# Kernel tuning notes

Measured on AMD Instinct MI355X. Metric: run time of the kernel, lower is better.

The kernel has to match this reference:

```python
import jax, jax.numpy as jnp
import numpy as np

HEADS = 16
DIM_HEAD = 64
MAX_REL_POS = 16  # temporal_length


def setup_inputs() -> dict:
    key = jax.random.key(0)
    ks = jax.random.split(key, 8)
    B, T, D = 2048, 16, 1024
    inner = HEADS * DIM_HEAD  # 1024
    w = 0.02  # weight init scale for numerical stability
    return {
        "x": jax.random.normal(ks[0], (B, T, D), jnp.float32),
        "Wq": jax.random.normal(ks[1], (inner, D), jnp.float32) * w,
        "Wk": jax.random.normal(ks[2], (inner, D), jnp.float32) * w,
        "Wv": jax.random.normal(ks[3], (inner, D), jnp.float32) * w,
        "Wo": jax.random.normal(ks[4], (D, inner), jnp.float32) * w,
        "bo": jnp.zeros((D,), jnp.float32),
        "rel_k_table": jax.random.normal(ks[5], (2 * MAX_REL_POS + 1, DIM_HEAD), jnp.float32) * w,
        "rel_v_table": jax.random.normal(ks[6], (2 * MAX_REL_POS + 1, DIM_HEAD), jnp.float32) * w,
    }


def reference(x, Wq, Wk, Wv, Wo, bo, rel_k_table, rel_v_table):
    B, T, D = x.shape
    h, dh = HEADS, DIM_HEAD
    scale = dh ** -0.5

    def split_heads(t):  # [B,T,h*dh] -> [B*h,T,dh]
        return t.reshape(B, T, h, dh).transpose(0, 2, 1, 3).reshape(B * h, T, dh)

    q = split_heads(x @ Wq.T)
    k = split_heads(x @ Wk.T)
    v = split_heads(x @ Wv.T)

    sim = jnp.einsum('bid,bjd->bij', q, k) * scale

    # relative-position bias: idx[i,j] = clip(j-i, -L, L) + L
    r = jnp.arange(T)
    idx = jnp.clip(r[None, :] - r[:, None], -MAX_REL_POS, MAX_REL_POS) + MAX_REL_POS
    k2 = rel_k_table[idx]  # [T,T,dh]
    sim = sim + jnp.einsum('btd,tsd->bts', q, k2) * scale

    attn = jax.nn.softmax(sim, axis=-1)
    out = jnp.einsum('bij,bjd->bid', attn, v)
    v2 = rel_v_table[idx]  # [T,T,dh]
    out = out + jnp.einsum('bts,tsd->btd', attn, v2)

    out = out.reshape(B, h, T, dh).transpose(0, 2, 1, 3).reshape(B, T, h * dh)
    return out @ Wo.T + bo
```

## Files before the change

### kernel.cpp

```cpp
#include <hip/hip_runtime.h>

#define HEADS 16
#define DIM_HEAD 64
#define T_SEQ 16
#define D_MODEL 1024
#define MAX_REL 16

typedef _Float16 half8 __attribute__((ext_vector_type(8)));
typedef float f32x4 __attribute__((ext_vector_type(4)));

__global__ __launch_bounds__(256)
void cvt_f32_f16(const float* __restrict__ in, _Float16* __restrict__ out, int n8) {
  int i = blockIdx.x * blockDim.x + threadIdx.x;
  if (i >= n8) return;
  float4 a = ((const float4*)in)[2 * i];
  float4 b = ((const float4*)in)[2 * i + 1];
  half8 h;
  h[0] = (_Float16)a.x; h[1] = (_Float16)a.y;
  h[2] = (_Float16)a.z; h[3] = (_Float16)a.w;
  h[4] = (_Float16)b.x; h[5] = (_Float16)b.y;
  h[6] = (_Float16)b.z; h[7] = (_Float16)b.w;
  ((half8*)out)[i] = h;
}

__global__ __launch_bounds__(256)
void prep_tables(const float* __restrict__ relk, const float* __restrict__ relv,
                 _Float16* __restrict__ RKh, _Float16* __restrict__ RVth) {
  const int i = threadIdx.x;
  {
    int m = i >> 3, d0 = (i & 7) * 8;
    float4 a = *(const float4*)(relk + m * 64 + d0);
    float4 b = *(const float4*)(relk + m * 64 + d0 + 4);
    half8 h;
    h[0] = (_Float16)a.x; h[1] = (_Float16)a.y;
    h[2] = (_Float16)a.z; h[3] = (_Float16)a.w;
    h[4] = (_Float16)b.x; h[5] = (_Float16)b.y;
    h[6] = (_Float16)b.z; h[7] = (_Float16)b.w;
    *(half8*)(RKh + m * 64 + d0) = h;
  }
  {
    int d = i >> 2, m0 = (i & 3) * 8;
    half8 h;
#pragma unroll
    for (int e = 0; e < 8; ++e) h[e] = (_Float16)relv[(m0 + e) * 64 + d];
    *(half8*)(RVth + d * 32 + m0) = h;
  }
}

__device__ __forceinline__ void gload_lds16(const _Float16* g, _Float16* l) {
  __builtin_amdgcn_global_load_lds(
      (const __attribute__((address_space(1))) unsigned int*)(uintptr_t)g,
      (__attribute__((address_space(3))) unsigned int*)(uintptr_t)l, 16, 0, 0);
}

template <bool OUT_F16>
__global__ __launch_bounds__(512, 2)
void gemm256(const _Float16* __restrict__ A, const _Float16* __restrict__ B,
             const float* __restrict__ bias, void* __restrict__ Cv,
             int M, int N, int K) {
  __shared__ _Float16 lds[2][2][2][128][64];
  const int tid = threadIdx.x;
  const int wave = tid >> 6, lane = tid & 63;
  const int wm = wave >> 2, wn = wave & 3;

  const int GN = N >> 8;
  const int nwg = gridDim.x;
  const int q = nwg >> 3, r = nwg & 7;
  const int xcd = blockIdx.x & 7, pos = blockIdx.x >> 3;
  const int wgid = (xcd < r ? xcd * (q + 1) : r * (q + 1) + (xcd - r) * q) + pos;
  const int bm = wgid / GN, bn = wgid % GN;

  const int fr = lane & 15;
  const int q4 = lane >> 4;
  const int l3 = lane >> 3;
  const int sl = (lane & 7) ^ l3;

  const _Float16* Ag = A + (size_t)(bm * 256) * K;
  const _Float16* Bg = B + (size_t)(bn * 256) * K;

  f32x4 acc[8][4];
#pragma unroll
  for (int m = 0; m < 8; ++m)
#pragma unroll
    for (int n = 0; n < 4; ++n) acc[m][n] = (f32x4){0.f, 0.f, 0.f, 0.f};

  auto stage_half = [&](int buf, int ab, int half, const _Float16* G, int k0) {
#pragma unroll
    for (int i = 0; i < 2; ++i) {
      int g = wave * 2 + i;
      const _Float16* src =
          G + (size_t)(half * 128 + g * 8 + l3) * K + k0 + sl * 8;
      gload_lds16(src, &lds[buf][ab][half][g * 8][0]);
    }
  };

  auto ldA = [&](int buf, int mf, int ks) {
    unsigned off = (unsigned)((mf * 16 + fr) * 128 + (ks * 4 + q4) * 16) ^
                   (unsigned)((fr & 7) << 4);
    return *(const half8*)((const char*)&lds[buf][0][wm][0][0] + off);
  };
  auto ldB = [&](int buf, int nf, int ks) {
    int rowB = wn * 64 + nf * 16 + fr;
    unsigned off = (unsigned)((rowB & 127) * 128 + (ks * 4 + q4) * 16) ^
                   (unsigned)((fr & 7) << 4);
    return *(const half8*)((const char*)&lds[buf][1][rowB >> 7][0][0] + off);
  };

#pragma unroll
  for (int h = 0; h < 2; ++h) {
    stage_half(0, 0, h, Ag, 0);
    stage_half(0, 1, h, Bg, 0);
  }
  asm volatile("s_waitcnt vmcnt(0)" ::: "memory");
  __builtin_amdgcn_s_barrier();

  const int NT = K >> 6;
  for (int t = 0; t < NT; ++t) {
    const int cur = t & 1, nxt = cur ^ 1;
    const bool pf = (t + 1 < NT);
    const int k1 = (t + 1) << 6;
    half8 bF[4][2];
#pragma unroll
    for (int p = 0; p < 4; ++p) {
      half8 aF[2][2];
#pragma unroll
      for (int i = 0; i < 2; ++i)
#pragma unroll
        for (int ks = 0; ks < 2; ++ks) aF[i][ks] = ldA(cur, p * 2 + i, ks);
      if (p == 0) {
#pragma unroll
        for (int nf = 0; nf < 4; ++nf)
#pragma unroll
          for (int ks = 0; ks < 2; ++ks) bF[nf][ks] = ldB(cur, nf, ks);
      }
      if (pf) {
        if (p < 2) stage_half(nxt, 0, p, Ag, k1);
        else       stage_half(nxt, 1, p - 2, Bg, k1);
      }
      asm volatile("s_waitcnt lgkmcnt(0)" ::: "memory");
      __builtin_amdgcn_sched_barrier(0);
      __builtin_amdgcn_s_setprio(1);
#pragma unroll
      for (int i = 0; i < 2; ++i)
#pragma unroll
        for (int nf = 0; nf < 4; ++nf)
#pragma unroll
          for (int ks = 0; ks < 2; ++ks)
            acc[p * 2 + i][nf] = __builtin_amdgcn_mfma_f32_16x16x32_f16(
                aF[i][ks], bF[nf][ks], acc[p * 2 + i][nf], 0, 0, 0);
      __builtin_amdgcn_s_setprio(0);
      __builtin_amdgcn_sched_barrier(0);
      if (p == 3) asm volatile("s_waitcnt vmcnt(0)" ::: "memory");
      __builtin_amdgcn_s_barrier();
    }
  }

  const int row_l = q4 * 4;
#pragma unroll
  for (int mf = 0; mf < 8; ++mf) {
#pragma unroll
    for (int nf = 0; nf < 4; ++nf) {
      int col = bn * 256 + wn * 64 + nf * 16 + fr;
#pragma unroll
      for (int r4 = 0; r4 < 4; ++r4) {
        int row = bm * 256 + wm * 128 + mf * 16 + row_l + r4;
        if (OUT_F16) {
          ((_Float16*)Cv)[(size_t)row * N + col] = (_Float16)acc[mf][nf][r4];
        } else {
          ((float*)Cv)[(size_t)row * N + col] = acc[mf][nf][r4] + bias[col];
        }
      }
    }
  }
}

__global__ __launch_bounds__(256)
void attn_mfma(const _Float16* __restrict__ QKV,
               const _Float16* __restrict__ RKh, const _Float16* __restrict__ RVth,
               _Float16* __restrict__ O) {
  __shared__ _Float16 PB[4][16][72];
  __shared__ _Float16 VtP[4][64][40];

  const int tid = threadIdx.x;
  const int wave = tid >> 6, lane = tid & 63;

#pragma unroll
  for (int z = 0; z < 6; ++z) {
    int idx = z * 64 + lane;
    int row = idx / 24, cd = idx % 24;
    *(unsigned int*)&PB[wave][row][16 + 2 * cd] = 0u;
  }
#pragma unroll
  for (int z = 0; z < 8; ++z) {
    int idx = z * 64 + lane;
    int row = idx >> 3, cd = idx & 7;
    *(unsigned int*)&VtP[wave][row][16 + 2 * cd] = 0u;
  }

  const int bh = blockIdx.x * 4 + wave;
  const int b = bh >> 4, h = bh & 15;
  const size_t qbase = (size_t)(b * T_SEQ) * 3072 + h * 64;
  const int fr = lane & 15, fk8 = (lane >> 4) * 8;

  half8 aQ0 = *(const half8*)(QKV + qbase + (size_t)fr * 3072 + fk8);
  half8 aQ1 = *(const half8*)(QKV + qbase + (size_t)fr * 3072 + 32 + fk8);
  half8 bK0 = *(const half8*)(QKV + qbase + 1024 + (size_t)fr * 3072 + fk8);
  half8 bK1 = *(const half8*)(QKV + qbase + 1024 + (size_t)fr * 3072 + 32 + fk8);

  half8 rk0a = *(const half8*)(RKh + fr * 64 + fk8);
  half8 rk0b = *(const half8*)(RKh + fr * 64 + 32 + fk8);
  half8 rk1a = *(const half8*)(RKh + (16 + fr) * 64 + fk8);
  half8 rk1b = *(const half8*)(RKh + (16 + fr) * 64 + 32 + fk8);

  {
    const _Float16* vp = QKV + qbase + 2048 + (size_t)fr * 3072 + (lane >> 4) * 16;
    half8 v0 = *(const half8*)vp;
    half8 v1 = *(const half8*)(vp + 8);
    int d0 = (lane >> 4) * 16;
#pragma unroll
    for (int e = 0; e < 8; ++e) VtP[wave][d0 + e][fr] = v0[e];
#pragma unroll
    for (int e = 0; e < 8; ++e) VtP[wave][d0 + 8 + e][fr] = v1[e];
  }

  f32x4 accS = {0.f, 0.f, 0.f, 0.f};
  accS = __builtin_amdgcn_mfma_f32_16x16x32_f16(aQ0, bK0, accS, 0, 0, 0);
  accS = __builtin_amdgcn_mfma_f32_16x16x32_f16(aQ1, bK1, accS, 0, 0, 0);

  f32x4 G0 = {0.f, 0.f, 0.f, 0.f}, G1 = {0.f, 0.f, 0.f, 0.f};
  G0 = __builtin_amdgcn_mfma_f32_16x16x32_f16(aQ0, rk0a, G0, 0, 0, 0);
  G0 = __builtin_amdgcn_mfma_f32_16x16x32_f16(aQ1, rk0b, G0, 0, 0, 0);
  G1 = __builtin_amdgcn_mfma_f32_16x16x32_f16(aQ0, rk1a, G1, 0, 0, 0);
  G1 = __builtin_amdgcn_mfma_f32_16x16x32_f16(aQ1, rk1b, G1, 0, 0, 0);

  const int ibase = (lane >> 4) * 4;
#pragma unroll
  for (int r = 0; r < 4; ++r) {
    const int i = ibase + r;
    const int ridx = fr - i + MAX_REL;
    const int src = (lane & 48) | (ridx & 15);
    float g0 = __shfl(G0[r], src);
    float g1 = __shfl(G1[r], src);
    float g = (ridx >= 16) ? g1 : g0;
    float s = (accS[r] + g) * 0.125f;
    float mx = s;
#pragma unroll
    for (int w = 8; w >= 1; w >>= 1) mx = fmaxf(mx, __shfl_xor(mx, w));
    float e = __expf(s - mx);
    float sum = e;
#pragma unroll
    for (int w = 8; w >= 1; w >>= 1) sum += __shfl_xor(sum, w);
    _Float16 ph = (_Float16)(e / sum);
    PB[wave][i][fr] = ph;
    PB[wave][i][32 + (fr - i + MAX_REL)] = ph;
  }

  half8 aP0 = *(const half8*)&PB[wave][fr][fk8];
  half8 aP1 = *(const half8*)&PB[wave][fr][32 + fk8];
  const size_t obase = (size_t)(b * T_SEQ) * D_MODEL + h * 64;
#pragma unroll
  for (int t = 0; t < 4; ++t) {
    half8 bv = *(const half8*)&VtP[wave][t * 16 + fr][fk8];
    half8 br = *(const half8*)(RVth + (t * 16 + fr) * 32 + fk8);
    f32x4 o = {0.f, 0.f, 0.f, 0.f};
    o = __builtin_amdgcn_mfma_f32_16x16x32_f16(aP0, bv, o, 0, 0, 0);
    o = __builtin_amdgcn_mfma_f32_16x16x32_f16(aP1, br, o, 0, 0, 0);
#pragma unroll
    for (int r = 0; r < 4; ++r)
      O[obase + (size_t)(ibase + r) * D_MODEL + t * 16 + fr] = (_Float16)o[r];
  }
}

extern "C" void kernel_launch(void* const* d_in, const int* in_sizes, int n_in,
                              void* d_out, int out_size, void* d_ws, size_t ws_size,
                              hipStream_t stream) {
  const float* x  = (const float*)d_in[0];
  const float* Wq = (const float*)d_in[1];
  const float* Wk = (const float*)d_in[2];
  const float* Wv = (const float*)d_in[3];
  const float* Wo = (const float*)d_in[4];
  const float* bo = (const float*)d_in[5];
  const float* rk = (const float*)d_in[6];
  const float* rv = (const float*)d_in[7];
  float* out = (float*)d_out;

  const int total_rows = 2048 * T_SEQ;
  const size_t wsz = (size_t)D_MODEL * D_MODEL;

  _Float16* Wqkvh = (_Float16*)d_ws;
  _Float16* Woh  = Wqkvh + 3 * wsz;
  _Float16* RKh  = Woh + wsz;
  _Float16* RVth = RKh + 2048;
  _Float16* chunk_base = RVth + 2048;

  {
    int n8 = (int)(wsz / 8);
    int blocks = (n8 + 255) / 256;
    cvt_f32_f16<<<blocks, 256, 0, stream>>>(Wq, Wqkvh, n8);
    cvt_f32_f16<<<blocks, 256, 0, stream>>>(Wk, Wqkvh + wsz, n8);
    cvt_f32_f16<<<blocks, 256, 0, stream>>>(Wv, Wqkvh + 2 * wsz, n8);
    cvt_f32_f16<<<blocks, 256, 0, stream>>>(Wo, Woh, n8);
    prep_tables<<<1, 256, 0, stream>>>(rk, rv, RKh, RVth);
  }

  const size_t per_row_bytes = (size_t)5120 * sizeof(_Float16);
  size_t avail = ws_size - (size_t)(4 * wsz + 4096) * sizeof(_Float16);
  size_t rows_fit = avail / per_row_bytes;
  int rows_c = (rows_fit > (size_t)total_rows) ? total_rows : (int)rows_fit;
  rows_c = (rows_c / 256) * 256;
  if (rows_c < 256) rows_c = 256;

  for (int r0 = 0; r0 < total_rows; r0 += rows_c) {
    int rc = total_rows - r0;
    if (rc > rows_c) rc = rows_c;

    _Float16* xh   = chunk_base;
    _Float16* QKVb = xh + (size_t)rows_c * 1024;
    _Float16* AO   = QKVb + (size_t)rows_c * 3072;

    {
      int n8 = rc * 128;
      cvt_f32_f16<<<(n8 + 255) / 256, 256, 0, stream>>>(
          x + (size_t)r0 * D_MODEL, xh, n8);
    }

    gemm256<true><<<(3072 / 256) * (rc / 256), 512, 0, stream>>>(
        xh, Wqkvh, nullptr, QKVb, rc, 3072, 1024);

    attn_mfma<<<rc / 4, 256, 0, stream>>>(QKVb, RKh, RVth, AO);

    gemm256<false><<<(1024 / 256) * (rc / 256), 512, 0, stream>>>(
        AO, Woh, bo, out + (size_t)r0 * D_MODEL, rc, 1024, 1024);
  }
}
```

Baseline: 420.0 us.

## Issue whole-tile prefetch up front and double-buffer A fragments across MFMA phases

Restructures the GEMM main loop so the global-to-LDS prefetch of the entire next K tile is issued at the start of each iteration rather than split across four phases. A fragments are ping-ponged between two register sets so LDS reads for the next quarter overlap MFMA of the current quarter. The explicit lgkmcnt waits and sched_barriers are removed, leaving the compiler to schedule LDS waits. This adds register pressure and relies on compiler scheduling, which may reduce occupancy or interleave poorly.

Result: slower. 440.0 us (+4.8%).

```diff
diff --git a/kernel.cpp b/kernel.cpp
--- a/kernel.cpp
+++ b/kernel.cpp
@@ -93,6 +93,12 @@
       gload_lds16(src, &lds[buf][ab][half][g * 8][0]);
     }
   };
+  auto stage_tile = [&](int buf, int k0) {
+    stage_half(buf, 0, 0, Ag, k0);
+    stage_half(buf, 0, 1, Ag, k0);
+    stage_half(buf, 1, 0, Bg, k0);
+    stage_half(buf, 1, 1, Bg, k0);
+  };
 
   auto ldA = [&](int buf, int mf, int ks) {
     unsigned off = (unsigned)((mf * 16 + fr) * 128 + (ks * 4 + q4) * 16) ^
@@ -106,11 +112,33 @@
     return *(const half8*)((const char*)&lds[buf][1][rowB >> 7][0][0] + off);
   };
 
-#pragma unroll
-  for (int h = 0; h < 2; ++h) {
-    stage_half(0, 0, h, Ag, 0);
-    stage_half(0, 1, h, Bg, 0);
-  }
+  half8 bF[4][2], aA[2][2], aB[2][2];
+  auto rdA = [&](half8 (&dst)[2][2], int buf, int qd) {
+#pragma unroll
+    for (int i = 0; i < 2; ++i)
+#pragma unroll
+      for (int ks = 0; ks < 2; ++ks) dst[i][ks] = ldA(buf, qd * 2 + i, ks);
+  };
+  auto rdB = [&](int buf) {
+#pragma unroll
+    for (int nf = 0; nf < 4; ++nf)
+#pragma unroll
+      for (int ks = 0; ks < 2; ++ks) bF[nf][ks] = ldB(buf, nf, ks);
+  };
+  auto mm = [&](int p, half8 (&af)[2][2]) {
+    __builtin_amdgcn_s_setprio(1);
+#pragma unroll
+    for (int i = 0; i < 2; ++i)
+#pragma unroll
+      for (int nf = 0; nf < 4; ++nf)
+#pragma unroll
+        for (int ks = 0; ks < 2; ++ks)
+          acc[p * 2 + i][nf] = __builtin_amdgcn_mfma_f32_16x16x32_f16(
+              af[i][ks], bF[nf][ks], acc[p * 2 + i][nf], 0, 0, 0);
+    __builtin_amdgcn_s_setprio(0);
+  };
+
+  stage_tile(0, 0);
   asm volatile("s_waitcnt vmcnt(0)" ::: "memory");
   __builtin_amdgcn_s_barrier();
 
@@ -119,40 +147,25 @@
     const int cur = t & 1, nxt = cur ^ 1;
     const bool pf = (t + 1 < NT);
     const int k1 = (t + 1) << 6;
-    half8 bF[4][2];
-#pragma unroll
-    for (int p = 0; p < 4; ++p) {
-      half8 aF[2][2];
-#pragma unroll
-      for (int i = 0; i < 2; ++i)
-#pragma unroll
-        for (int ks = 0; ks < 2; ++ks) aF[i][ks] = ldA(cur, p * 2 + i, ks);
-      if (p == 0) {
-#pragma unroll
-        for (int nf = 0; nf < 4; ++nf)
-#pragma unroll
-          for (int ks = 0; ks < 2; ++ks) bF[nf][ks] = ldB(cur, nf, ks);
-      }
-      if (pf) {
-        if (p < 2) stage_half(nxt, 0, p, Ag, k1);
-        else       stage_half(nxt, 1, p - 2, Bg, k1);
-      }
-      asm volatile("s_waitcnt lgkmcnt(0)" ::: "memory");
-      __builtin_amdgcn_sched_barrier(0);
-      __builtin_amdgcn_s_setprio(1);
-#pragma unroll
-      for (int i = 0; i < 2; ++i)
-#pragma unroll
-        for (int nf = 0; nf < 4; ++nf)
-#pragma unroll
-          for (int ks = 0; ks < 2; ++ks)
-            acc[p * 2 + i][nf] = __builtin_amdgcn_mfma_f32_16x16x32_f16(
-                aF[i][ks], bF[nf][ks], acc[p * 2 + i][nf], 0, 0, 0);
-      __builtin_amdgcn_s_setprio(0);
-      __builtin_amdgcn_sched_barrier(0);
-      if (p == 3) asm volatile("s_waitcnt vmcnt(0)" ::: "memory");
-      __builtin_amdgcn_s_barrier();
-    }
+
+    if (pf) stage_tile(nxt, k1);
+    rdB(cur);
+    rdA(aA, cur, 0);
+    rdA(aB, cur, 1);
+    mm(0, aA);
+    __builtin_amdgcn_s_barrier();
+
+    rdA(aA, cur, 2);
+    mm(1, aB);
+    __builtin_amdgcn_s_barrier();
+
+    rdA(aB, cur, 3);
+    mm(2, aA);
+    __builtin_amdgcn_s_barrier();
+
+    mm(3, aB);
+    if (pf) asm volatile("s_waitcnt vmcnt(0)" ::: "memory");
+    __builtin_amdgcn_s_barrier();
   }
 
   const int row_l = q4 * 4;
```

## Reorder GEMM prefetch by consumption order and relax vmcnt waits

Applied to the files above, without the earlier changes.

Splits the staging of the next K tile into 8-row groups. B and the A rows needed first are issued early, and the rest of A is spread across the four compute phases. The per-iteration full vmcnt(0) drain becomes partial waits (vmcnt(2), vmcnt(3)), so late A loads can still be in flight while the first MFMA phases of the next iteration run. The ordering is fragile: correctness depends on the group-to-wave mapping and the wait counts matching exactly.

After: 416.1 us. No clear change (-0.9%).

```diff
diff --git a/kernel.cpp b/kernel.cpp
--- a/kernel.cpp
+++ b/kernel.cpp
@@ -84,15 +84,11 @@
 #pragma unroll
     for (int n = 0; n < 4; ++n) acc[m][n] = (f32x4){0.f, 0.f, 0.f, 0.f};
 
-  auto stage_half = [&](int buf, int ab, int half, const _Float16* G, int k0) {
-#pragma unroll
-    for (int i = 0; i < 2; ++i) {
-      int g = wave * 2 + i;
-      const _Float16* src =
-          G + (size_t)(half * 128 + g * 8 + l3) * K + k0 + sl * 8;
-      gload_lds16(src, &lds[buf][ab][half][g * 8][0]);
-    }
+  auto stage_group = [&](int buf, int ab, int g, const _Float16* G, int k0) {
+    const _Float16* src = G + (size_t)(g * 8 + l3) * K + k0 + sl * 8;
+    gload_lds16(src, &lds[buf][ab][g >> 4][(g & 15) * 8][0]);
   };
+  auto lateg = [&](int idx) { return idx < 12 ? 4 + idx : 8 + idx; };
 
   auto ldA = [&](int buf, int mf, int ks) {
     unsigned off = (unsigned)((mf * 16 + fr) * 128 + (ks * 4 + q4) * 16) ^
@@ -106,11 +102,25 @@
     return *(const half8*)((const char*)&lds[buf][1][rowB >> 7][0][0] + off);
   };
 
-#pragma unroll
-  for (int h = 0; h < 2; ++h) {
-    stage_half(0, 0, h, Ag, 0);
-    stage_half(0, 1, h, Bg, 0);
-  }
+  half8 bF[4][2];
+  auto mm = [&](int p, half8 (&af)[2][2]) {
+    __builtin_amdgcn_s_setprio(1);
+#pragma unroll
+    for (int i = 0; i < 2; ++i)
+#pragma unroll
+      for (int nf = 0; nf < 4; ++nf)
+#pragma unroll
+        for (int ks = 0; ks < 2; ++ks)
+          acc[p * 2 + i][nf] = __builtin_amdgcn_mfma_f32_16x16x32_f16(
+              af[i][ks], bF[nf][ks], acc[p * 2 + i][nf], 0, 0, 0);
+    __builtin_amdgcn_s_setprio(0);
+  };
+
+#pragma unroll
+  for (int j = 0; j < 4; ++j) stage_group(0, 1, wave * 4 + j, Bg, 0);
+  stage_group(0, 0, wave < 4 ? wave : wave + 12, Ag, 0);
+#pragma unroll
+  for (int j = 0; j < 3; ++j) stage_group(0, 0, lateg(3 * wave + j), Ag, 0);
   asm volatile("s_waitcnt vmcnt(0)" ::: "memory");
   __builtin_amdgcn_s_barrier();
 
@@ -119,40 +129,70 @@
     const int cur = t & 1, nxt = cur ^ 1;
     const bool pf = (t + 1 < NT);
     const int k1 = (t + 1) << 6;
-    half8 bF[4][2];
-#pragma unroll
-    for (int p = 0; p < 4; ++p) {
-      half8 aF[2][2];
-#pragma unroll
-      for (int i = 0; i < 2; ++i)
-#pragma unroll
-        for (int ks = 0; ks < 2; ++ks) aF[i][ks] = ldA(cur, p * 2 + i, ks);
-      if (p == 0) {
-#pragma unroll
-        for (int nf = 0; nf < 4; ++nf)
-#pragma unroll
-          for (int ks = 0; ks < 2; ++ks) bF[nf][ks] = ldB(cur, nf, ks);
-      }
-      if (pf) {
-        if (p < 2) stage_half(nxt, 0, p, Ag, k1);
-        else       stage_half(nxt, 1, p - 2, Bg, k1);
-      }
-      asm volatile("s_waitcnt lgkmcnt(0)" ::: "memory");
-      __builtin_amdgcn_sched_barrier(0);
-      __builtin_amdgcn_s_setprio(1);
-#pragma unroll
-      for (int i = 0; i < 2; ++i)
-#pragma unroll
-        for (int nf = 0; nf < 4; ++nf)
-#pragma unroll
-          for (int ks = 0; ks < 2; ++ks)
-            acc[p * 2 + i][nf] = __builtin_amdgcn_mfma_f32_16x16x32_f16(
-                aF[i][ks], bF[nf][ks], acc[p * 2 + i][nf], 0, 0, 0);
-      __builtin_amdgcn_s_setprio(0);
-      __builtin_amdgcn_sched_barrier(0);
-      if (p == 3) asm volatile("s_waitcnt vmcnt(0)" ::: "memory");
-      __builtin_amdgcn_s_barrier();
-    }
+    half8 aF[2][2];
+
+#pragma unroll
+    for (int nf = 0; nf < 4; ++nf)
+#pragma unroll
+      for (int ks = 0; ks < 2; ++ks) bF[nf][ks] = ldB(cur, nf, ks);
+#pragma unroll
+    for (int i = 0; i < 2; ++i)
+#pragma unroll
+      for (int ks = 0; ks < 2; ++ks) aF[i][ks] = ldA(cur, i, ks);
+    if (pf) {
+      stage_group(nxt, 1, wave * 4 + 0, Bg, k1);
+      stage_group(nxt, 1, wave * 4 + 1, Bg, k1);
+    }
+    asm volatile("s_waitcnt lgkmcnt(0)" ::: "memory");
+    __builtin_amdgcn_sched_barrier(0);
+    mm(0, aF);
+    __builtin_amdgcn_sched_barrier(0);
+    if (pf) asm volatile("s_waitcnt vmcnt(2)" ::: "memory");
+    else    asm volatile("s_waitcnt vmcnt(0)" ::: "memory");
+    __builtin_amdgcn_s_barrier();
+
+#pragma unroll
+    for (int i = 0; i < 2; ++i)
+#pragma unroll
+      for (int ks = 0; ks < 2; ++ks) aF[i][ks] = ldA(cur, 2 + i, ks);
+    if (pf) {
+      stage_group(nxt, 1, wave * 4 + 2, Bg, k1);
+      stage_group(nxt, 1, wave * 4 + 3, Bg, k1);
+    }
+    asm volatile("s_waitcnt lgkmcnt(0)" ::: "memory");
+    __builtin_amdgcn_sched_barrier(0);
+    mm(1, aF);
+    __builtin_amdgcn_sched_barrier(0);
+    __builtin_amdgcn_s_barrier();
+
+#pragma unroll
+    for (int i = 0; i < 2; ++i)
+#pragma unroll
+      for (int ks = 0; ks < 2; ++ks) aF[i][ks] = ldA(cur, 4 + i, ks);
+    if (pf) {
+      stage_group(nxt, 0, wave < 4 ? wave : wave + 12, Ag, k1);
+      stage_group(nxt, 0, lateg(3 * wave + 0), Ag, k1);
+    }
+    asm volatile("s_waitcnt lgkmcnt(0)" ::: "memory");
+    __builtin_amdgcn_sched_barrier(0);
+    mm(2, aF);
+    __builtin_amdgcn_sched_barrier(0);
+    __builtin_amdgcn_s_barrier();
+
+#pragma unroll
+    for (int i = 0; i < 2; ++i)
+#pragma unroll
+      for (int ks = 0; ks < 2; ++ks) aF[i][ks] = ldA(cur, 6 + i, ks);
+    if (pf) {
+      stage_group(nxt, 0, lateg(3 * wave + 1), Ag, k1);
+      stage_group(nxt, 0, lateg(3 * wave + 2), Ag, k1);
+    }
+    asm volatile("s_waitcnt lgkmcnt(0)" ::: "memory");
+    __builtin_amdgcn_sched_barrier(0);
+    mm(3, aF);
+    __builtin_amdgcn_sched_barrier(0);
+    if (pf) asm volatile("s_waitcnt vmcnt(3)" ::: "memory");
+    __builtin_amdgcn_s_barrier();
   }
 
   const int row_l = q4 * 4;
```
